# Kernel optimization log

Hardware: AMD Instinct MI355X
Metric: run time of the kernel (lower is better)

## Reference

```python
import math
import jax, jax.numpy as jnp
import numpy as np

B, T = 2, 2048
D_MODEL, D_HEAD = 2048, 128
N_Q, N_KV = 16, 4
QPG = N_Q // N_KV  # queries per kv group
ROPE_BASE = 10000.0
YARN_SCALE = 4.0
ORIG_MAX_LEN = 4096
BETA_FAST, BETA_SLOW = 32.0, 1.0
RMS_EPS = 1.1920929e-07  # torch.finfo(float32).eps (nn.RMSNorm default)


def _yarn_inv_freq():
    inv = 1.0 / ROPE_BASE ** (np.arange(0, D_HEAD, 2, dtype=np.float32) / D_HEAD)
    wavelengths = 2.0 * math.pi / inv
    low_wavelen = ORIG_MAX_LEN / BETA_SLOW
    high_wavelen = ORIG_MAX_LEN / BETA_FAST
    gamma = np.clip((low_wavelen - wavelengths) / (low_wavelen - high_wavelen), 0.0, 1.0)
    return (gamma * inv + (1.0 - gamma) * inv / YARN_SCALE).astype(np.float32)

INV_FREQ = jnp.asarray(_yarn_inv_freq())  # (D_HEAD//2,) constant buffer
MSCALE = 0.1 * math.log(YARN_SCALE) + 1.0
ATTN_SCALE = 1.0 / (MSCALE * math.sqrt(D_HEAD))


def _rms_norm(x, w):
    # normalize over last dim (d_head), learnable per-dim weight
    return x * jax.lax.rsqrt(jnp.mean(x * x, axis=-1, keepdims=True) + RMS_EPS) * w


def _apply_rope(x):
    # x: (..., T, d_head)
    t = jnp.arange(x.shape[-2], dtype=jnp.float32)
    freqs = jnp.outer(t, INV_FREQ)                 # (T, d/2)
    emb = jnp.concatenate([freqs, freqs], axis=-1)  # (T, d)
    cos, sin = jnp.cos(emb), jnp.sin(emb)
    half = x.shape[-1] // 2
    x_rot = jnp.concatenate([-x[..., half:], x[..., :half]], axis=-1)
    return x * cos + x_rot * sin


def setup_inputs() -> dict:
    key = jax.random.key(0)
    ks = jax.random.split(key, 5)
    x = jax.random.normal(ks[0], (B, T, D_MODEL), dtype=jnp.float32)
    w_scale = 0.02
    Wq = jax.random.normal(ks[1], (D_MODEL, N_Q * D_HEAD), dtype=jnp.float32) * w_scale
    Wkv = jax.random.normal(ks[2], (D_MODEL, 2 * N_KV * D_HEAD), dtype=jnp.float32) * w_scale
    Wo = jax.random.normal(ks[3], (N_Q * D_HEAD, D_MODEL), dtype=jnp.float32) * w_scale
    q_norm_w = jnp.ones((D_HEAD,), dtype=jnp.float32)
    k_norm_w = jnp.ones((D_HEAD,), dtype=jnp.float32)
    return {"x": x, "Wq": Wq, "Wkv": Wkv, "Wo": Wo,
            "q_norm_w": q_norm_w, "k_norm_w": k_norm_w}


def reference(x, Wq, Wkv, Wo, q_norm_w, k_norm_w):
    b, t, _ = x.shape
    # projections
    q = (x @ Wq).reshape(b, t, QPG, N_KV, D_HEAD).transpose(0, 2, 3, 1, 4)  # (b,qpg,g,t,d)
    kv = x @ Wkv
    k, v = jnp.split(kv, 2, axis=-1)
    k = k.reshape(b, t, N_KV, D_HEAD).transpose(0, 2, 1, 3)  # (b,g,t,d)
    v = v.reshape(b, t, N_KV, D_HEAD).transpose(0, 2, 1, 3)  # (b,g,t,d)
    # RMSNorm + YaRN RoPE on q,k (math done in float32 as in source)
    q = _apply_rope(_rms_norm(q, q_norm_w))
    k = _apply_rope(_rms_norm(k, k_norm_w))
    # GQA replication: head index h = qpg*N_KV + g (matches source rearrange/reshape)
    q = q.reshape(b, N_Q, t, D_HEAD)
    k = jnp.broadcast_to(k[:, None], (b, QPG, N_KV, t, D_HEAD)).reshape(b, N_Q, t, D_HEAD)
    v = jnp.broadcast_to(v[:, None], (b, QPG, N_KV, t, D_HEAD)).reshape(b, N_Q, t, D_HEAD)
    # causal SDPA with custom scale
    scores = jnp.einsum('bhtd,bhsd->bhts', q, k) * ATTN_SCALE
    causal = jnp.tril(jnp.ones((t, t), dtype=bool))
    scores = jnp.where(causal, scores, jnp.finfo(scores.dtype).min)
    probs = jax.nn.softmax(scores, axis=-1)
    attn = jnp.einsum('bhts,bhsd->bhtd', probs, v)
    out = attn.transpose(0, 2, 1, 3).reshape(b, t, N_Q * D_HEAD)
    return out @ Wo
```

## Files before the change

kernel.cpp:

```cpp
#include <hip/hip_runtime.h>
#include <cmath>

typedef float f32x4 __attribute__((ext_vector_type(4)));
typedef __bf16 bf16x8 __attribute__((ext_vector_type(8)));

#define DEV static __device__ __forceinline__

DEV unsigned short f2bf(float f) {
  unsigned int u = __builtin_bit_cast(unsigned int, f);
  u += 0x7FFFu + ((u >> 16) & 1u);
  return (unsigned short)(u >> 16);
}
DEV float bf2f(unsigned short h) {
  unsigned int u = ((unsigned int)h) << 16;
  return __builtin_bit_cast(float, u);
}
DEV f32x4 mfma16(bf16x8 a, bf16x8 b, f32x4 c) {
  return __builtin_amdgcn_mfma_f32_16x16x32_bf16(a, b, c, 0, 0, 0);
}
DEV void dma16(const void* g, void* l) {
  __builtin_amdgcn_global_load_lds(
      (const __attribute__((address_space(1))) void*)(uintptr_t)g,
      (__attribute__((address_space(3))) void*)(unsigned int)(uintptr_t)l,
      16, 0, 0);
}

constexpr int T_SEQ = 2048;

__global__ __launch_bounds__(256) void build_rope(float2* __restrict__ rope) {
  int gid = blockIdx.x * 256 + threadIdx.x;
  if (gid >= T_SEQ * 64) return;
  int t = gid >> 6, i = gid & 63;
  double inv = pow(10000.0, -((double)(2 * i)) / 128.0);
  double wl = 6.283185307179586 / inv;
  double gm = (4096.0 - wl) / (4096.0 - 128.0);
  gm = gm < 0.0 ? 0.0 : (gm > 1.0 ? 1.0 : gm);
  float f = (float)(gm * inv + (1.0 - gm) * inv * 0.25);
  float th = (float)t * f;
  float s, c;
  sincosf(th, &s, &c);
  rope[gid] = make_float2(c, s);
}

__global__ __launch_bounds__(256) void cvt_f32_bf16(const float4* __restrict__ in,
                                                    ushort* __restrict__ out, int n4) {
  int i = blockIdx.x * 256 + threadIdx.x;
  if (i >= n4) return;
  float4 v = in[i];
  unsigned int lo = (unsigned int)f2bf(v.x) | ((unsigned int)f2bf(v.y) << 16);
  unsigned int hi = (unsigned int)f2bf(v.z) | ((unsigned int)f2bf(v.w) << 16);
  int row = i >> 9;
  int e = (i * 4) & 2047;
  size_t o = ((size_t)row << 11) + (size_t)(e ^ ((row & 7) << 3));
  *(uint2*)(out + o) = make_uint2(lo, hi);
}

__global__ __launch_bounds__(256) void tconv(const float* __restrict__ in,
                                             ushort* __restrict__ out, int R, int C) {
  __shared__ ushort tile[64][65];
  int c0 = blockIdx.x * 64, r0 = blockIdx.y * 64;
  int j = threadIdx.x & 63, i0 = threadIdx.x >> 6;
#pragma unroll
  for (int ii = 0; ii < 16; ++ii) {
    int i = i0 + ii * 4;
    tile[i][j] = f2bf(in[(size_t)(r0 + i) * C + c0 + j]);
  }
  __syncthreads();
#pragma unroll
  for (int ii = 0; ii < 16; ++ii) {
    int jr = i0 + ii * 4;
    out[(size_t)(c0 + jr) * R + ((r0 + j) ^ ((jr & 7) << 3))] = tile[j][jr];
  }
}

template <int OUT_BF16>
__global__ __launch_bounds__(256) void gemm_bt(const ushort* __restrict__ A,
                                               const ushort* __restrict__ Bt,
                                               void* __restrict__ Cv,
                                               int M, int N, int K) {
  __shared__ ushort lA[128 * 64];
  __shared__ ushort lB[128 * 64];
  const int tid = threadIdx.x;
  const int lane = tid & 63;
  const int w = tid >> 6;
  const int m0 = blockIdx.y * 128;
  const int n0 = blockIdx.x * 128;
  const int wm = (w >> 1) << 6;
  const int wn = (w & 1) << 6;

  f32x4 acc[4][4] = {};

  const size_t K2 = (size_t)K * 2;
  const char* Ab = (const char*)A + (size_t)m0 * K2;
  const char* Bb = (const char*)Bt + (size_t)n0 * K2;
  const int drow = w * 32 + (lane >> 3);
  const int dcb = (lane & 7) * 16;

  for (int k0 = 0; k0 < K; k0 += 64) {
#pragma unroll
    for (int ii = 0; ii < 4; ++ii) {
      const int off = w * 4096 + ii * 1024;
      const size_t gofs = (size_t)(drow + ii * 8) * K2 + (size_t)k0 * 2 + dcb;
      dma16(Ab + gofs, (char*)lA + off);
      dma16(Bb + gofs, (char*)lB + off);
    }
    __syncthreads();
#pragma unroll
    for (int kc = 0; kc < 2; ++kc) {
      bf16x8 a[4], bb[4];
#pragma unroll
      for (int mt = 0; mt < 4; ++mt) {
        int row = wm + mt * 16 + (lane & 15);
        int byo = kc * 64 + ((lane >> 4) << 4);
        a[mt] = *(const bf16x8*)((const char*)lA + row * 128 + (byo ^ ((row & 7) << 4)));
      }
#pragma unroll
      for (int nt = 0; nt < 4; ++nt) {
        int row = wn + nt * 16 + (lane & 15);
        int byo = kc * 64 + ((lane >> 4) << 4);
        bb[nt] = *(const bf16x8*)((const char*)lB + row * 128 + (byo ^ ((row & 7) << 4)));
      }
#pragma unroll
      for (int mt = 0; mt < 4; ++mt)
#pragma unroll
        for (int nt = 0; nt < 4; ++nt)
          acc[mt][nt] = mfma16(a[mt], bb[nt], acc[mt][nt]);
    }
    __syncthreads();
  }

  const int rr = (lane >> 4) << 2;
  const int cc = lane & 15;
  if (OUT_BF16) {
    ushort* C = (ushort*)Cv;
#pragma unroll
    for (int mt = 0; mt < 4; ++mt)
#pragma unroll
      for (int nt = 0; nt < 4; ++nt)
#pragma unroll
        for (int j = 0; j < 4; ++j) {
          int r = m0 + wm + mt * 16 + rr + j;
          int c = n0 + wn + nt * 16 + cc;
          C[(size_t)r * N + c] = f2bf(acc[mt][nt][j]);
        }
  } else {
    float* C = (float*)Cv;
#pragma unroll
    for (int mt = 0; mt < 4; ++mt)
#pragma unroll
      for (int nt = 0; nt < 4; ++nt)
#pragma unroll
        for (int j = 0; j < 4; ++j) {
          int r = m0 + wm + mt * 16 + rr + j;
          int c = n0 + wn + nt * 16 + cc;
          C[(size_t)r * N + c] = acc[mt][nt][j];
        }
  }
}

__global__ __launch_bounds__(256) void norm_rope(const ushort* __restrict__ qkv,
                                                 const float* __restrict__ qw,
                                                 const float* __restrict__ kw,
                                                 const float2* __restrict__ rope,
                                                 ushort* __restrict__ qout,
                                                 ushort* __restrict__ kout,
                                                 float q_scale) {
  const int w = threadIdx.x >> 6, lane = threadIdx.x & 63;
  const int vi = blockIdx.x * 4 + w;
  const ushort* src;
  const float* wt;
  ushort* dst;
  float extra;
  int t, bb;
  if (vi < 65536) {
    int row = vi >> 4, H = vi & 15;
    bb = row >> 11;
    t = row & 2047;
    src = qkv + (size_t)row * 3072 + H * 128 + lane * 2;
    wt = qw;
    extra = q_scale;
    dst = qout + ((size_t)(bb * 16 + H) * T_SEQ + t) * 128 + lane * 2;
  } else {
    int vi2 = vi - 65536;
    int row = vi2 >> 2, gg = vi2 & 3;
    bb = row >> 11;
    t = row & 2047;
    src = qkv + (size_t)row * 3072 + 2048 + gg * 128 + lane * 2;
    wt = kw;
    extra = 1.f;
    dst = kout + ((size_t)(bb * 4 + gg) * T_SEQ + t) * 128 +
          ((lane * 2) ^ ((t & 7) << 3));
  }
  float x0 = bf2f(src[0]), x1 = bf2f(src[1]);
  float ss = x0 * x0 + x1 * x1;
#pragma unroll
  for (int d = 1; d < 64; d <<= 1) ss += __shfl_xor(ss, d, 64);
  float sc = rsqrtf(ss * (1.f / 128.f) + 1.1920929e-7f);
  float w0 = wt[lane * 2], w1 = wt[lane * 2 + 1];
  float xn0 = x0 * sc * w0, xn1 = x1 * sc * w1;
  float p0 = __shfl_xor(xn0, 32, 64), p1 = __shfl_xor(xn1, 32, 64);
  float r0 = lane < 32 ? -p0 : p0;
  float r1 = lane < 32 ? -p1 : p1;
  int i0 = (lane * 2) & 63;
  float2 cs0 = rope[t * 64 + i0];
  float2 cs1 = rope[t * 64 + i0 + 1];
  float o0 = (xn0 * cs0.x + r0 * cs0.y) * extra;
  float o1 = (xn1 * cs1.x + r1 * cs1.y) * extra;
  unsigned int pk = (unsigned int)f2bf(o0) | ((unsigned int)f2bf(o1) << 16);
  *(unsigned int*)dst = pk;
}

__global__ __launch_bounds__(256) void tv_kernel(const ushort* __restrict__ qkv,
                                                 ushort* __restrict__ vt) {
  __shared__ ushort tile[64][65];
  int t0 = blockIdx.x * 64;
  int y = blockIdx.y;
  int dh = y & 1, bg = y >> 1;
  int bb = bg >> 2, g = bg & 3;
  int j = threadIdx.x & 63, i0 = threadIdx.x >> 6;
#pragma unroll
  for (int ii = 0; ii < 16; ++ii) {
    int i = i0 + ii * 4;
    tile[i][j] = qkv[(size_t)(bb * T_SEQ + t0 + i) * 3072 + 2560 + g * 128 + dh * 64 + j];
  }
  __syncthreads();
#pragma unroll
  for (int ii = 0; ii < 16; ++ii) {
    int jr = i0 + ii * 4;
    vt[((size_t)bg * 128 + dh * 64 + jr) * T_SEQ + ((t0 + j) ^ ((jr & 7) << 3))] = tile[j][jr];
  }
}

__global__ __launch_bounds__(512, 4) void attn_fwd(const ushort* __restrict__ qh,
                                                   const ushort* __restrict__ kh,
                                                   const ushort* __restrict__ vt,
                                                   ushort* __restrict__ o) {
  const int f = blockIdx.x;
  const int half = f >> 8, c = f & 255;
  const int kk = c >> 5, bh = c & 31;
  const int qt = half ? kk : (15 - kk);
  const int b = bh >> 4, H = bh & 15;
  const int g = H & 3;
  const int tid = threadIdx.x, lane = tid & 63, w = tid >> 6;
  const int wrow0 = qt * 128 + w * 16;

  __shared__ ushort lK[2][64 * 128];
  __shared__ ushort lV[2][128 * 64];
  __shared__ ushort lP[8 * 16 * 64];

  bf16x8 qf[4];
  {
    const ushort* qb = qh + ((size_t)(b * 16 + H) * T_SEQ + wrow0 + (lane & 15)) * 128 +
                       ((lane >> 4) << 3);
#pragma unroll
    for (int kc = 0; kc < 4; ++kc) qf[kc] = *(const bf16x8*)(qb + kc * 32);
  }

  f32x4 oacc[8] = {};
  float mrow = -INFINITY, lrow = 0.f;

  const char* kpl = (const char*)(kh + (size_t)(b * 4 + g) * T_SEQ * 128);
  const char* vpl = (const char*)(vt + (size_t)(b * 4 + g) * 128 * T_SEQ);

  auto stage = [&](int j, int bi) {
#pragma unroll
    for (int ii = 0; ii < 2; ++ii) {
      const int off = w * 2048 + ii * 1024;
      dma16(kpl + (size_t)j * 16384 + off + lane * 16, (char*)lK[bi] + off);
      const int vrow = w * 16 + ii * 8 + (lane >> 3);
      dma16(vpl + (size_t)vrow * (T_SEQ * 2) + j * 128 + (lane & 7) * 16,
            (char*)lV[bi] + off);
    }
  };

  stage(0, 0);

  const int qrow = wrow0 + (lane & 15);
  const int rsel = ((lane >> 4) << 2);

  const int jmax = 2 * qt + 1;
  for (int j = 0; j <= jmax; ++j) {
    const int cur = j & 1;
    if (j < jmax) {
      stage(j + 1, cur ^ 1);
      asm volatile("s_waitcnt vmcnt(4)" ::: "memory");
    } else {
      asm volatile("s_waitcnt vmcnt(0)" ::: "memory");
    }
    __builtin_amdgcn_s_barrier();
    __builtin_amdgcn_sched_barrier(0);

    f32x4 s[4];
#pragma unroll
    for (int nt = 0; nt < 4; ++nt) {
      bf16x8 kf[4];
      int krow = nt * 16 + (lane & 15);
#pragma unroll
      for (int kc = 0; kc < 4; ++kc) {
        int byo = kc * 64 + ((lane >> 4) << 4);
        kf[kc] = *(const bf16x8*)((const char*)lK[cur] + krow * 256 + (byo ^ ((krow & 7) << 4)));
      }
      f32x4 a = {0.f, 0.f, 0.f, 0.f};
#pragma unroll
      for (int kc = 0; kc < 4; ++kc) a = mfma16(kf[kc], qf[kc], a);
      s[nt] = a;
    }

    if (j * 64 + 63 > wrow0) {
#pragma unroll
      for (int nt = 0; nt < 4; ++nt)
#pragma unroll
        for (int jj = 0; jj < 4; ++jj) {
          int col = j * 64 + nt * 16 + ((lane >> 4) << 2) + jj;
          if (col > qrow) s[nt][jj] = -3.0e38f;
        }
    }

    float pm0 = fmaxf(fmaxf(s[0][0], s[0][1]), fmaxf(s[0][2], s[0][3]));
    float pm1 = fmaxf(fmaxf(s[1][0], s[1][1]), fmaxf(s[1][2], s[1][3]));
    float pm2 = fmaxf(fmaxf(s[2][0], s[2][1]), fmaxf(s[2][2], s[2][3]));
    float pm3 = fmaxf(fmaxf(s[3][0], s[3][1]), fmaxf(s[3][2], s[3][3]));
    float pm = fmaxf(fmaxf(pm0, pm1), fmaxf(pm2, pm3));
    pm = fmaxf(pm, __shfl_xor(pm, 16, 64));
    pm = fmaxf(pm, __shfl_xor(pm, 32, 64));

    float mn = mrow;
    if (!__all(pm <= mrow + 11.5417f)) {
      mn = fmaxf(mrow, pm);
      float rsc = exp2f(mrow - mn);
      mrow = mn;
      lrow *= rsc;
      float rr0 = __shfl(rsc, rsel + 0, 64);
      float rr1 = __shfl(rsc, rsel + 1, 64);
      float rr2 = __shfl(rsc, rsel + 2, 64);
      float rr3 = __shfl(rsc, rsel + 3, 64);
#pragma unroll
      for (int dt = 0; dt < 8; ++dt) {
        oacc[dt][0] *= rr0; oacc[dt][1] *= rr1;
        oacc[dt][2] *= rr2; oacc[dt][3] *= rr3;
      }
    }

    float ps = 0.f;
#pragma unroll
    for (int nt = 0; nt < 4; ++nt) {
      float p0 = exp2f(s[nt][0] - mn);
      float p1 = exp2f(s[nt][1] - mn);
      float p2 = exp2f(s[nt][2] - mn);
      float p3 = exp2f(s[nt][3] - mn);
      ps += (p0 + p1) + (p2 + p3);
      unsigned int w0 = (unsigned int)f2bf(p0) | ((unsigned int)f2bf(p1) << 16);
      unsigned int w1 = (unsigned int)f2bf(p2) | ((unsigned int)f2bf(p3) << 16);
      int prow = lane & 15;
      int pcb = (nt * 32 + ((lane >> 4) << 3)) ^ ((prow & 7) << 4);
      *(uint2*)((char*)lP + w * 2048 + prow * 128 + pcb) = make_uint2(w0, w1);
    }
    ps += __shfl_xor(ps, 16, 64);
    ps += __shfl_xor(ps, 32, 64);
    lrow += ps;

#pragma unroll
    for (int kc2 = 0; kc2 < 2; ++kc2) {
      int prow = lane & 15;
      int pbo = kc2 * 64 + ((lane >> 4) << 4);
      bf16x8 pa = *(const bf16x8*)((char*)lP + w * 2048 + prow * 128 +
                                   (pbo ^ ((prow & 7) << 4)));
#pragma unroll
      for (int dt = 0; dt < 8; ++dt) {
        int vrow = dt * 16 + (lane & 15);
        int vbo = kc2 * 64 + ((lane >> 4) << 4);
        bf16x8 vf = *(const bf16x8*)((const char*)lV[cur] + vrow * 128 + (vbo ^ ((vrow & 7) << 4)));
        oacc[dt] = mfma16(pa, vf, oacc[dt]);
      }
    }

    __builtin_amdgcn_sched_barrier(0);
    __builtin_amdgcn_s_barrier();
  }

  float linv = 1.f / lrow;
  float iv0 = __shfl(linv, rsel + 0, 64);
  float iv1 = __shfl(linv, rsel + 1, 64);
  float iv2 = __shfl(linv, rsel + 2, 64);
  float iv3 = __shfl(linv, rsel + 3, 64);
#pragma unroll
  for (int dt = 0; dt < 8; ++dt) {
    float v0 = oacc[dt][0] * iv0, v1 = oacc[dt][1] * iv1;
    float v2 = oacc[dt][2] * iv2, v3 = oacc[dt][3] * iv3;
    int col = H * 128 + dt * 16 + (lane & 15);
    int row = wrow0 + rsel;
    o[(size_t)(b * T_SEQ + row + 0) * 2048 + (col ^ (((row + 0) & 7) << 3))] = f2bf(v0);
    o[(size_t)(b * T_SEQ + row + 1) * 2048 + (col ^ (((row + 1) & 7) << 3))] = f2bf(v1);
    o[(size_t)(b * T_SEQ + row + 2) * 2048 + (col ^ (((row + 2) & 7) << 3))] = f2bf(v2);
    o[(size_t)(b * T_SEQ + row + 3) * 2048 + (col ^ (((row + 3) & 7) << 3))] = f2bf(v3);
  }
}

extern "C" void kernel_launch(void* const* d_in, const int* in_sizes, int n_in,
                              void* d_out, int out_size, void* d_ws, size_t ws_size,
                              hipStream_t stream) {
  (void)in_sizes; (void)n_in; (void)out_size; (void)ws_size;
  const float* x = (const float*)d_in[0];
  const float* Wq = (const float*)d_in[1];
  const float* Wkv = (const float*)d_in[2];
  const float* Wo = (const float*)d_in[3];
  const float* qnw = (const float*)d_in[4];
  const float* knw = (const float*)d_in[5];
  float* out = (float*)d_out;
  char* ws = (char*)d_ws;

  ushort* xb = (ushort*)(ws);
  ushort* wqkv = (ushort*)(ws + 16777216);
  ushort* wot = (ushort*)(ws + 29360128);
  ushort* qkvraw = (ushort*)(ws + 37748736);
  ushort* kh = (ushort*)(ws + 62914560);
  ushort* vtp = (ushort*)(ws + 67108864);
  float2* rope = (float2*)(ws + 71303168);
  ushort* qh = xb;
  ushort* attnb = qkvraw;

  float attn_scale = 1.0f / ((0.1f * logf(4.0f) + 1.0f) * sqrtf(128.0f));
  float q_scale = attn_scale * 1.44269504f;

  build_rope<<<512, 256, 0, stream>>>(rope);
  cvt_f32_bf16<<<8192, 256, 0, stream>>>((const float4*)x, xb, 2097152);
  tconv<<<dim3(32, 32), 256, 0, stream>>>(Wq, wqkv, 2048, 2048);
  tconv<<<dim3(16, 32), 256, 0, stream>>>(Wkv, wqkv + (size_t)2048 * 2048, 2048, 1024);
  tconv<<<dim3(32, 32), 256, 0, stream>>>(Wo, wot, 2048, 2048);
  gemm_bt<1><<<dim3(24, 32), 256, 0, stream>>>(xb, wqkv, qkvraw, 4096, 3072, 2048);
  norm_rope<<<20480, 256, 0, stream>>>(qkvraw, qnw, knw, rope, qh, kh, q_scale);
  tv_kernel<<<dim3(32, 16), 256, 0, stream>>>(qkvraw, vtp);
  attn_fwd<<<512, 512, 0, stream>>>(qh, kh, vtp, attnb);
  gemm_bt<0><<<dim3(16, 32), 256, 0, stream>>>(attnb, wot, out, 4096, 2048, 2048);
}
```

Before: 229.4 us.

## Switch attention to 32x32 MFMA with register-resident P via permlane swap

Rewrites the attention kernel to use 32x32x16 bf16 MFMA tiles, with each of 4 waves owning 32 query rows instead of 8 waves owning 16 each. The probabilities P are converted and rearranged in registers with v_cvt_pk_bf16_f32 and v_permlane32_swap, so they no longer go through LDS. Wave priority is raised around the MFMA sections. The aim is fewer LDS round trips and shuffles per tile and higher MFMA efficiency. The cost is more registers per wave and fewer waves per block, which may reduce latency hiding.

```diff
diff --git a/kernel.cpp b/kernel.cpp
--- a/kernel.cpp
+++ b/kernel.cpp
@@ -2,6 +2,7 @@
 #include <cmath>
 
 typedef float f32x4 __attribute__((ext_vector_type(4)));
+typedef float f32x16 __attribute__((ext_vector_type(16)));
 typedef __bf16 bf16x8 __attribute__((ext_vector_type(8)));
 
 #define DEV static __device__ __forceinline__
@@ -15,8 +16,16 @@
   unsigned int u = ((unsigned int)h) << 16;
   return __builtin_bit_cast(float, u);
 }
+DEV unsigned int cvtpk(float lo, float hi) {
+  unsigned int r;
+  asm("v_cvt_pk_bf16_f32 %0, %1, %2" : "=v"(r) : "v"(lo), "v"(hi));
+  return r;
+}
 DEV f32x4 mfma16(bf16x8 a, bf16x8 b, f32x4 c) {
   return __builtin_amdgcn_mfma_f32_16x16x32_bf16(a, b, c, 0, 0, 0);
+}
+DEV f32x16 mfma32(bf16x8 a, bf16x8 b, f32x16 c) {
+  return __builtin_amdgcn_mfma_f32_32x32x16_bf16(a, b, c, 0, 0, 0);
 }
 DEV void dma16(const void* g, void* l) {
   __builtin_amdgcn_global_load_lds(
@@ -231,7 +240,19 @@
   }
 }
 
-__global__ __launch_bounds__(512, 4) void attn_fwd(const ushort* __restrict__ qh,
+#define MKPA(P, B)                                                      \
+  ({                                                                    \
+    unsigned X1 = cvtpk(P[B + 0], P[B + 1]);                            \
+    unsigned X2 = cvtpk(P[B + 2], P[B + 3]);                            \
+    unsigned Y1 = cvtpk(P[B + 4], P[B + 5]);                            \
+    unsigned Y2 = cvtpk(P[B + 6], P[B + 7]);                            \
+    asm("v_permlane32_swap_b32 %0, %1" : "+v"(X1), "+v"(Y1));           \
+    asm("v_permlane32_swap_b32 %0, %1" : "+v"(X2), "+v"(Y2));           \
+    uint4 u4 = {X1, X2, Y1, Y2};                                        \
+    __builtin_bit_cast(bf16x8, u4);                                     \
+  })
+
+__global__ __launch_bounds__(256, 2) void attn_fwd(const ushort* __restrict__ qh,
                                                    const ushort* __restrict__ kh,
                                                    const ushort* __restrict__ vt,
                                                    ushort* __restrict__ o) {
@@ -242,21 +263,21 @@
   const int b = bh >> 4, H = bh & 15;
   const int g = H & 3;
   const int tid = threadIdx.x, lane = tid & 63, w = tid >> 6;
-  const int wrow0 = qt * 128 + w * 16;
+  const int hi = lane >> 5;
+  const int ql = lane & 31;
+  const int wrow0 = qt * 128 + w * 32;
 
   __shared__ ushort lK[2][64 * 128];
   __shared__ ushort lV[2][128 * 64];
-  __shared__ ushort lP[8 * 16 * 64];
-
-  bf16x8 qf[4];
+
+  bf16x8 qf[8];
   {
-    const ushort* qb = qh + ((size_t)(b * 16 + H) * T_SEQ + wrow0 + (lane & 15)) * 128 +
-                       ((lane >> 4) << 3);
-#pragma unroll
-    for (int kc = 0; kc < 4; ++kc) qf[kc] = *(const bf16x8*)(qb + kc * 32);
-  }
-
-  f32x4 oacc[8] = {};
+    const ushort* qb = qh + ((size_t)(b * 16 + H) * T_SEQ + wrow0 + ql) * 128 + 8 * hi;
+#pragma unroll
+    for (int cc = 0; cc < 8; ++cc) qf[cc] = *(const bf16x8*)(qb + 16 * cc);
+  }
+
+  f32x16 oacc[4] = {};
   float mrow = -INFINITY, lrow = 0.f;
 
   const char* kpl = (const char*)(kh + (size_t)(b * 4 + g) * T_SEQ * 128);
@@ -264,10 +285,10 @@
 
   auto stage = [&](int j, int bi) {
 #pragma unroll
-    for (int ii = 0; ii < 2; ++ii) {
-      const int off = w * 2048 + ii * 1024;
+    for (int ii = 0; ii < 4; ++ii) {
+      const int off = w * 4096 + ii * 1024;
       dma16(kpl + (size_t)j * 16384 + off + lane * 16, (char*)lK[bi] + off);
-      const int vrow = w * 16 + ii * 8 + (lane >> 3);
+      const int vrow = w * 32 + ii * 8 + (lane >> 3);
       dma16(vpl + (size_t)vrow * (T_SEQ * 2) + j * 128 + (lane & 7) * 16,
             (char*)lV[bi] + off);
     }
@@ -275,53 +296,54 @@
 
   stage(0, 0);
 
-  const int qrow = wrow0 + (lane & 15);
-  const int rsel = ((lane >> 4) << 2);
-
+  const int swK = (ql & 7) << 4;
   const int jmax = 2 * qt + 1;
+
   for (int j = 0; j <= jmax; ++j) {
     const int cur = j & 1;
     if (j < jmax) {
       stage(j + 1, cur ^ 1);
-      asm volatile("s_waitcnt vmcnt(4)" ::: "memory");
+      asm volatile("s_waitcnt vmcnt(8)" ::: "memory");
     } else {
       asm volatile("s_waitcnt vmcnt(0)" ::: "memory");
     }
     __builtin_amdgcn_s_barrier();
     __builtin_amdgcn_sched_barrier(0);
 
-    f32x4 s[4];
-#pragma unroll
-    for (int nt = 0; nt < 4; ++nt) {
-      bf16x8 kf[4];
-      int krow = nt * 16 + (lane & 15);
-#pragma unroll
-      for (int kc = 0; kc < 4; ++kc) {
-        int byo = kc * 64 + ((lane >> 4) << 4);
-        kf[kc] = *(const bf16x8*)((const char*)lK[cur] + krow * 256 + (byo ^ ((krow & 7) << 4)));
+    const char* lKc = (const char*)lK[cur];
+    const char* lVc = (const char*)lV[cur];
+
+    f32x16 s0 = {}, s1 = {};
+    __builtin_amdgcn_s_setprio(1);
+#pragma unroll
+    for (int cc = 0; cc < 8; ++cc) {
+      bf16x8 kf = *(const bf16x8*)(lKc + ql * 256 + ((32 * cc + 16 * hi) ^ swK));
+      s0 = mfma32(kf, qf[cc], s0);
+    }
+#pragma unroll
+    for (int cc = 0; cc < 8; ++cc) {
+      bf16x8 kf = *(const bf16x8*)(lKc + (32 + ql) * 256 + ((32 * cc + 16 * hi) ^ swK));
+      s1 = mfma32(kf, qf[cc], s1);
+    }
+    __builtin_amdgcn_s_setprio(0);
+
+    if (j * 64 + 63 > wrow0) {
+      const int q = wrow0 + ql;
+      const int kvb = j * 64 + 4 * hi;
+#pragma unroll
+      for (int r = 0; r < 16; ++r) {
+        const int kv0 = kvb + (r & 3) + 8 * (r >> 2);
+        if (kv0 > q) s0[r] = -3.0e38f;
+        if (kv0 + 32 > q) s1[r] = -3.0e38f;
       }
-      f32x4 a = {0.f, 0.f, 0.f, 0.f};
-#pragma unroll
-      for (int kc = 0; kc < 4; ++kc) a = mfma16(kf[kc], qf[kc], a);
-      s[nt] = a;
-    }
-
-    if (j * 64 + 63 > wrow0) {
-#pragma unroll
-      for (int nt = 0; nt < 4; ++nt)
-#pragma unroll
-        for (int jj = 0; jj < 4; ++jj) {
-          int col = j * 64 + nt * 16 + ((lane >> 4) << 2) + jj;
-          if (col > qrow) s[nt][jj] = -3.0e38f;
-        }
-    }
-
-    float pm0 = fmaxf(fmaxf(s[0][0], s[0][1]), fmaxf(s[0][2], s[0][3]));
-    float pm1 = fmaxf(fmaxf(s[1][0], s[1][1]), fmaxf(s[1][2], s[1][3]));
-    float pm2 = fmaxf(fmaxf(s[2][0], s[2][1]), fmaxf(s[2][2], s[2][3]));
-    float pm3 = fmaxf(fmaxf(s[3][0], s[3][1]), fmaxf(s[3][2], s[3][3]));
-    float pm = fmaxf(fmaxf(pm0, pm1), fmaxf(pm2, pm3));
-    pm = fmaxf(pm, __shfl_xor(pm, 16, 64));
+    }
+
+    float tm[8];
+#pragma unroll
+    for (int r = 0; r < 8; ++r)
+      tm[r] = fmaxf(fmaxf(s0[r], s0[r + 8]), fmaxf(s1[r], s1[r + 8]));
+    float pm = fmaxf(fmaxf(fmaxf(tm[0], tm[1]), fmaxf(tm[2], tm[3])),
+                     fmaxf(fmaxf(tm[4], tm[5]), fmaxf(tm[6], tm[7])));
     pm = fmaxf(pm, __shfl_xor(pm, 32, 64));
 
     float mn = mrow;
@@ -330,69 +352,64 @@
       float rsc = exp2f(mrow - mn);
       mrow = mn;
       lrow *= rsc;
-      float rr0 = __shfl(rsc, rsel + 0, 64);
-      float rr1 = __shfl(rsc, rsel + 1, 64);
-      float rr2 = __shfl(rsc, rsel + 2, 64);
-      float rr3 = __shfl(rsc, rsel + 3, 64);
-#pragma unroll
-      for (int dt = 0; dt < 8; ++dt) {
-        oacc[dt][0] *= rr0; oacc[dt][1] *= rr1;
-        oacc[dt][2] *= rr2; oacc[dt][3] *= rr3;
+#pragma unroll
+      for (int r = 0; r < 16; ++r) {
+        float rv = __shfl(rsc, (r & 3) + 8 * (r >> 2) + 4 * hi, 64);
+#pragma unroll
+        for (int n = 0; n < 4; ++n) oacc[n][r] *= rv;
       }
     }
 
-    float ps = 0.f;
-#pragma unroll
-    for (int nt = 0; nt < 4; ++nt) {
-      float p0 = exp2f(s[nt][0] - mn);
-      float p1 = exp2f(s[nt][1] - mn);
-      float p2 = exp2f(s[nt][2] - mn);
-      float p3 = exp2f(s[nt][3] - mn);
-      ps += (p0 + p1) + (p2 + p3);
-      unsigned int w0 = (unsigned int)f2bf(p0) | ((unsigned int)f2bf(p1) << 16);
-      unsigned int w1 = (unsigned int)f2bf(p2) | ((unsigned int)f2bf(p3) << 16);
-      int prow = lane & 15;
-      int pcb = (nt * 32 + ((lane >> 4) << 3)) ^ ((prow & 7) << 4);
-      *(uint2*)((char*)lP + w * 2048 + prow * 128 + pcb) = make_uint2(w0, w1);
-    }
-    ps += __shfl_xor(ps, 16, 64);
+    f32x16 p0, p1;
+#pragma unroll
+    for (int r = 0; r < 16; ++r) {
+      p0[r] = exp2f(s0[r] - mn);
+      p1[r] = exp2f(s1[r] - mn);
+    }
+    float ta[8];
+#pragma unroll
+    for (int r = 0; r < 8; ++r) ta[r] = (p0[r] + p0[r + 8]) + (p1[r] + p1[r + 8]);
+    float ps = ((ta[0] + ta[1]) + (ta[2] + ta[3])) + ((ta[4] + ta[5]) + (ta[6] + ta[7]));
     ps += __shfl_xor(ps, 32, 64);
     lrow += ps;
 
-#pragma unroll
-    for (int kc2 = 0; kc2 < 2; ++kc2) {
-      int prow = lane & 15;
-      int pbo = kc2 * 64 + ((lane >> 4) << 4);
-      bf16x8 pa = *(const bf16x8*)((char*)lP + w * 2048 + prow * 128 +
-                                   (pbo ^ ((prow & 7) << 4)));
-#pragma unroll
-      for (int dt = 0; dt < 8; ++dt) {
-        int vrow = dt * 16 + (lane & 15);
-        int vbo = kc2 * 64 + ((lane >> 4) << 4);
-        bf16x8 vf = *(const bf16x8*)((const char*)lV[cur] + vrow * 128 + (vbo ^ ((vrow & 7) << 4)));
-        oacc[dt] = mfma16(pa, vf, oacc[dt]);
-      }
-    }
+    bf16x8 pa0 = MKPA(p0, 0), pa1 = MKPA(p0, 8);
+    bf16x8 pa2 = MKPA(p1, 0), pa3 = MKPA(p1, 8);
+
+    __builtin_amdgcn_s_setprio(1);
+#pragma unroll
+    for (int n = 0; n < 4; ++n) {
+      const int row = 32 * n + ql;
+      const int swV = (row & 7) << 4;
+      const char* vb = lVc + row * 128;
+      bf16x8 vf0 = *(const bf16x8*)(vb + ((16 * hi) ^ swV));
+      bf16x8 vf1 = *(const bf16x8*)(vb + ((32 + 16 * hi) ^ swV));
+      bf16x8 vf2 = *(const bf16x8*)(vb + ((64 + 16 * hi) ^ swV));
+      bf16x8 vf3 = *(const bf16x8*)(vb + ((96 + 16 * hi) ^ swV));
+      oacc[n] = mfma32(pa0, vf0, oacc[n]);
+      oacc[n] = mfma32(pa1, vf1, oacc[n]);
+      oacc[n] = mfma32(pa2, vf2, oacc[n]);
+      oacc[n] = mfma32(pa3, vf3, oacc[n]);
+    }
+    __builtin_amdgcn_s_setprio(0);
 
     __builtin_amdgcn_sched_barrier(0);
     __builtin_amdgcn_s_barrier();
   }
 
   float linv = 1.f / lrow;
-  float iv0 = __shfl(linv, rsel + 0, 64);
-  float iv1 = __shfl(linv, rsel + 1, 64);
-  float iv2 = __shfl(linv, rsel + 2, 64);
-  float iv3 = __shfl(linv, rsel + 3, 64);
-#pragma unroll
-  for (int dt = 0; dt < 8; ++dt) {
-    float v0 = oacc[dt][0] * iv0, v1 = oacc[dt][1] * iv1;
-    float v2 = oacc[dt][2] * iv2, v3 = oacc[dt][3] * iv3;
-    int col = H * 128 + dt * 16 + (lane & 15);
-    int row = wrow0 + rsel;
-    o[(size_t)(b * T_SEQ + row + 0) * 2048 + (col ^ (((row + 0) & 7) << 3))] = f2bf(v0);
-    o[(size_t)(b * T_SEQ + row + 1) * 2048 + (col ^ (((row + 1) & 7) << 3))] = f2bf(v1);
-    o[(size_t)(b * T_SEQ + row + 2) * 2048 + (col ^ (((row + 2) & 7) << 3))] = f2bf(v2);
-    o[(size_t)(b * T_SEQ + row + 3) * 2048 + (col ^ (((row + 3) & 7) << 3))] = f2bf(v3);
+#pragma unroll
+  for (int r = 0; r < 16; ++r) {
+    const int qrr = (r & 3) + 8 * (r >> 2) + 4 * hi;
+    float iv = __shfl(linv, qrr, 64);
+    const int row = wrow0 + qrr;
+    const size_t base = (size_t)(b * T_SEQ + row) * 2048;
+    const int sw = (row & 7) << 3;
+#pragma unroll
+    for (int n = 0; n < 4; ++n) {
+      int col = H * 128 + n * 32 + ql;
+      o[base + (col ^ sw)] = f2bf(oacc[n][r] * iv);
+    }
   }
 }
 
@@ -430,6 +447,6 @@
   gemm_bt<1><<<dim3(24, 32), 256, 0, stream>>>(xb, wqkv, qkvraw, 4096, 3072, 2048);
   norm_rope<<<20480, 256, 0, stream>>>(qkvraw, qnw, knw, rope, qh, kh, q_scale);
   tv_kernel<<<dim3(32, 16), 256, 0, stream>>>(qkvraw, vtp);
-  attn_fwd<<<512, 512, 0, stream>>>(qh, kh, vtp, attnb);
+  attn_fwd<<<512, 256, 0, stream>>>(qh, kh, vtp, attnb);
   gemm_bt<0><<<dim3(16, 32), 256, 0, stream>>>(attnb, wot, out, 4096, 2048, 2048);
 }
```

Result: no change. 228.6 us (-0.4%).
